# Kernel tuning notes

Measured on AMD Instinct MI355X. Metric: run time of the kernel, lower is better.

Reference implementation:

```python
import jax, jax.numpy as jnp
import numpy as np


def setup_inputs() -> dict:
    key = jax.random.key(0)
    k1, k2, k3, k4 = jax.random.split(key, 4)
    B, S, IN, OUT = 4, 2048, 4096, 4096
    x = jax.random.normal(k1, (B, S, IN), dtype=jnp.float32)
    # 4-bit signed range [-8, 7], stored widened (torch uses int8)
    weight_quantized = jax.random.randint(k2, (OUT, IN), -8, 8, dtype=jnp.int32)
    # per-output-row scale, positive and small (abs-max / 7 style)
    weight_scale = jax.random.uniform(k3, (OUT,), dtype=jnp.float32) * 0.01 + 1e-4
    bias = jax.random.normal(k4, (OUT,), dtype=jnp.float32) * 0.01
    return {"x": x, "weight_quantized": weight_quantized,
            "weight_scale": weight_scale, "bias": bias}


def reference(x, weight_quantized, weight_scale, bias):
    # dequantize: [OUT, IN] int -> fp32 scaled per output row
    w = weight_quantized.astype(jnp.float32) * weight_scale[:, None]
    # F.linear: x @ w.T + bias  -> [B, S, OUT]
    out = jnp.einsum('bsi,oi->bso', x, w) + bias
    return out
```

## Files before the change

### kernel.cpp

```cpp
#include <hip/hip_runtime.h>
#include <hip/hip_bf16.h>

typedef __bf16 bf16x4 __attribute__((ext_vector_type(4)));
typedef __bf16 bf16x8 __attribute__((ext_vector_type(8)));
typedef float  floatx4 __attribute__((ext_vector_type(4)));

#define AS1 __attribute__((address_space(1)))
#define AS3 __attribute__((address_space(3)))

__global__ __launch_bounds__(256)
void cvt_both8(const float* __restrict__ xin, const int* __restrict__ win,
               __bf16* __restrict__ xout, __bf16* __restrict__ wout,
               int nx8, int nw8)
{
    const int stride = gridDim.x * 256;
    const int total  = nx8 + nw8;
    for (int i = blockIdx.x * 256 + threadIdx.x; i < total; i += stride) {
        if (i < nx8) {
            const float4* p = reinterpret_cast<const float4*>(xin) + (size_t)i * 2;
            float4 a = p[0], b = p[1];
            bf16x8 h;
            h[0] = (__bf16)a.x; h[1] = (__bf16)a.y; h[2] = (__bf16)a.z; h[3] = (__bf16)a.w;
            h[4] = (__bf16)b.x; h[5] = (__bf16)b.y; h[6] = (__bf16)b.z; h[7] = (__bf16)b.w;
            reinterpret_cast<bf16x8*>(xout)[i] = h;
        } else {
            int j = i - nx8;
            const int4* p = reinterpret_cast<const int4*>(win) + (size_t)j * 2;
            int4 a = p[0], b = p[1];
            bf16x8 h;
            h[0] = (__bf16)(float)a.x; h[1] = (__bf16)(float)a.y;
            h[2] = (__bf16)(float)a.z; h[3] = (__bf16)(float)a.w;
            h[4] = (__bf16)(float)b.x; h[5] = (__bf16)(float)b.y;
            h[6] = (__bf16)(float)b.z; h[7] = (__bf16)(float)b.w;
            reinterpret_cast<bf16x8*>(wout)[j] = h;
        }
    }
}

#define BM2 256
#define BN2 256
#define BK2 64

template<int P>
__device__ __forceinline__ void phaseAB(const __bf16* cA, const bf16x8 (&bfr)[4][2],
                                        floatx4 (&acc)[8][4],
                                        int wm, int lm, int kq, int sw)
{
    bf16x8 af[2][2];
#pragma unroll
    for (int ii = 0; ii < 2; ++ii)
#pragma unroll
        for (int h = 0; h < 2; ++h)
            af[ii][h] = *reinterpret_cast<const bf16x8*>(
                &cA[(wm + (2 * P + ii) * 16 + lm) * BK2 + ((kq + h * 4) ^ sw) * 8]);
    __builtin_amdgcn_s_setprio(1);
#pragma unroll
    for (int h = 0; h < 2; ++h)
#pragma unroll
        for (int ii = 0; ii < 2; ++ii)
#pragma unroll
            for (int j = 0; j < 4; ++j)
                acc[2 * P + ii][j] = __builtin_amdgcn_mfma_f32_16x16x32_bf16(
                                         af[ii][h], bfr[j][h], acc[2 * P + ii][j], 0, 0, 0);
    __builtin_amdgcn_s_setprio(0);
}

__device__ __forceinline__ void phase3(const __bf16* cA, const __bf16* cBn,
                                       const bf16x8 (&bfr)[4][2], bf16x8 (&bfrN)[4][2],
                                       floatx4 (&acc)[8][4],
                                       int wm, int wn, int lm, int kq, int sw)
{
    bf16x8 af[2][2];
#pragma unroll
    for (int ii = 0; ii < 2; ++ii)
#pragma unroll
        for (int h = 0; h < 2; ++h)
            af[ii][h] = *reinterpret_cast<const bf16x8*>(
                &cA[(wm + (6 + ii) * 16 + lm) * BK2 + ((kq + h * 4) ^ sw) * 8]);
#pragma unroll
    for (int j = 0; j < 4; ++j)
#pragma unroll
        for (int h = 0; h < 2; ++h)
            bfrN[j][h] = *reinterpret_cast<const bf16x8*>(
                &cBn[(wn + j * 16 + lm) * BK2 + ((kq + h * 4) ^ sw) * 8]);
    __builtin_amdgcn_s_setprio(1);
#pragma unroll
    for (int h = 0; h < 2; ++h)
#pragma unroll
        for (int ii = 0; ii < 2; ++ii)
#pragma unroll
            for (int j = 0; j < 4; ++j)
                acc[6 + ii][j] = __builtin_amdgcn_mfma_f32_16x16x32_bf16(
                                     af[ii][h], bfr[j][h], acc[6 + ii][j], 0, 0, 0);
    __builtin_amdgcn_s_setprio(0);
}

#define BARRIER() asm volatile("s_barrier" ::: "memory")

__global__ __launch_bounds__(512)
void gemm_bf16_bt_pipe(const __bf16* __restrict__ A, const __bf16* __restrict__ B,
                       const float* __restrict__ scale, const float* __restrict__ bias,
                       float* __restrict__ Out, int M, int N, int K)
{
    __shared__ __bf16 sA[2][BM2 * BK2];
    __shared__ __bf16 sB[2][BN2 * BK2];

    const int tid  = threadIdx.x;
    const int wave = tid >> 6;
    const int lane = tid & 63;
    const int row0 = blockIdx.y * BM2;
    const int col0 = blockIdx.x * BN2;

    const int sRow = lane >> 3;
    const int gBlk = (lane & 7) ^ sRow;
    const size_t aBase = (size_t)(row0 + wave * 8 + sRow) * K + gBlk * 8;
    const size_t bBase = (size_t)(col0 + wave * 8 + sRow) * K + gBlk * 8;
    const int ldsWOff = wave * 8 * BK2;

#define STAGE_A(buf, q, kt_) \
    __builtin_amdgcn_global_load_lds( \
        (const AS1 void*)(A + aBase + (size_t)(q) * 64 * K + (size_t)(kt_) * BK2), \
        (AS3 void*)&sA[(buf)][(q) * 64 * BK2 + ldsWOff], 16, 0, 0)
#define STAGE_B(buf, q, kt_) \
    __builtin_amdgcn_global_load_lds( \
        (const AS1 void*)(B + bBase + (size_t)(q) * 64 * K + (size_t)(kt_) * BK2), \
        (AS3 void*)&sB[(buf)][(q) * 64 * BK2 + ldsWOff], 16, 0, 0)

    const int wm = (wave >> 2) * 128;
    const int wn = (wave & 3) * 64;
    const int lm = lane & 15;
    const int kq = lane >> 4;
    const int sw = lm & 7;

    floatx4 acc[8][4];
#pragma unroll
    for (int i = 0; i < 8; ++i)
#pragma unroll
        for (int j = 0; j < 4; ++j)
            acc[i][j] = (floatx4)0.0f;

    bf16x8 bfrA[4][2], bfrB[4][2];
    const int nt = K / BK2;

    STAGE_A(0, 0, 0); STAGE_A(0, 1, 0); STAGE_A(0, 2, 0); STAGE_A(0, 3, 0);
    STAGE_B(0, 0, 0); STAGE_B(0, 1, 0); STAGE_B(0, 2, 0); STAGE_B(0, 3, 0);
    STAGE_B(1, 0, 1); STAGE_B(1, 1, 1); STAGE_B(1, 2, 1); STAGE_B(1, 3, 1);
    STAGE_A(1, 0, 1); STAGE_A(1, 2, 1);
    asm volatile("s_waitcnt vmcnt(6)" ::: "memory");
    BARRIER();
#pragma unroll
    for (int j = 0; j < 4; ++j)
#pragma unroll
        for (int h = 0; h < 2; ++h)
            bfrA[j][h] = *reinterpret_cast<const bf16x8*>(
                &sB[0][(wn + j * 16 + lm) * BK2 + ((kq + h * 4) ^ sw) * 8]);

    for (int it = 0; it < nt / 2; ++it) {
        const int kt = 2 * it;
        const int n1 = kt + 1;
        const int n2 = (kt + 2 < nt) ? kt + 2 : 0;
        const int n3 = (kt + 3 < nt) ? kt + 3 : 0;

        STAGE_A(1, 1, n1); STAGE_A(1, 3, n1);
        phaseAB<0>(sA[0], bfrA, acc, wm, lm, kq, sw);
        BARRIER();
        STAGE_B(0, 0, n2); STAGE_B(0, 1, n2); STAGE_B(0, 2, n2); STAGE_B(0, 3, n2);
        phaseAB<1>(sA[0], bfrA, acc, wm, lm, kq, sw);
        BARRIER();
        STAGE_A(0, 0, n2); STAGE_A(0, 2, n2);
        phaseAB<2>(sA[0], bfrA, acc, wm, lm, kq, sw);
        asm volatile("s_waitcnt vmcnt(8)" ::: "memory");
        BARRIER();
        phase3(sA[0], sB[1], bfrA, bfrB, acc, wm, wn, lm, kq, sw);
        BARRIER();

        STAGE_A(0, 1, n2); STAGE_A(0, 3, n2);
        phaseAB<0>(sA[1], bfrB, acc, wm, lm, kq, sw);
        BARRIER();
        STAGE_B(1, 0, n3); STAGE_B(1, 1, n3); STAGE_B(1, 2, n3); STAGE_B(1, 3, n3);
        phaseAB<1>(sA[1], bfrB, acc, wm, lm, kq, sw);
        BARRIER();
        STAGE_A(1, 0, n3); STAGE_A(1, 2, n3);
        phaseAB<2>(sA[1], bfrB, acc, wm, lm, kq, sw);
        asm volatile("s_waitcnt vmcnt(8)" ::: "memory");
        BARRIER();
        phase3(sA[1], sB[0], bfrB, bfrA, acc, wm, wn, lm, kq, sw);
        BARRIER();
    }
    asm volatile("s_waitcnt vmcnt(0)" ::: "memory");

#pragma unroll
    for (int j = 0; j < 4; ++j) {
        int n = col0 + wn + j * 16 + lm;
        float sc = scale[n];
        float bi = bias[n];
#pragma unroll
        for (int i = 0; i < 8; ++i) {
#pragma unroll
            for (int r = 0; r < 4; ++r) {
                int m = row0 + wm + i * 16 + kq * 4 + r;
                Out[(size_t)m * N + n] = sc * acc[i][j][r] + bi;
            }
        }
    }
#undef STAGE_A
#undef STAGE_B
}

#define BM 128
#define BN 128
#define BK 64

__global__ __launch_bounds__(256)
void gemm_bf16_bt(const __bf16* __restrict__ A, const __bf16* __restrict__ B,
                  const float* __restrict__ scale, const float* __restrict__ bias,
                  float* __restrict__ Out, int M, int N, int K)
{
    __shared__ __bf16 sA[BM * BK];
    __shared__ __bf16 sB[BN * BK];

    const int tid  = threadIdx.x;
    const int row0 = blockIdx.y * BM;
    const int col0 = blockIdx.x * BN;
    const int wave = tid >> 6;
    const int lane = tid & 63;

    const int sRow = lane >> 3;
    const int gBlk = (lane & 7) ^ sRow;
    size_t aOff[4], bOff[4];
    const __bf16* ldsA[4];
    const __bf16* ldsB[4];
#pragma unroll
    for (int q = 0; q < 4; ++q) {
        int r = wave * 32 + q * 8 + sRow;
        aOff[q] = (size_t)(row0 + r) * K + gBlk * 8;
        bOff[q] = (size_t)(col0 + r) * K + gBlk * 8;
        ldsA[q] = &sA[(wave * 32 + q * 8) * BK];
        ldsB[q] = &sB[(wave * 32 + q * 8) * BK];
    }

    const int wm = (wave >> 1) * 64;
    const int wn = (wave & 1) * 64;
    const int lm = lane & 15;
    const int kq = lane >> 4;
    const int sw = lm & 7;

    floatx4 acc[4][4];
#pragma unroll
    for (int i = 0; i < 4; ++i)
#pragma unroll
        for (int j = 0; j < 4; ++j)
            acc[i][j] = (floatx4)0.0f;

    for (int k0 = 0; k0 < K; k0 += BK) {
#pragma unroll
        for (int q = 0; q < 4; ++q) {
            __builtin_amdgcn_global_load_lds((const AS1 void*)(A + aOff[q] + k0),
                                             (AS3 void*)ldsA[q], 16, 0, 0);
            __builtin_amdgcn_global_load_lds((const AS1 void*)(B + bOff[q] + k0),
                                             (AS3 void*)ldsB[q], 16, 0, 0);
        }
        __syncthreads();

#pragma unroll
        for (int h = 0; h < 2; ++h) {
            const int blkA = (kq + h * 4);
            bf16x8 af[4], bfr[4];
#pragma unroll
            for (int i = 0; i < 4; ++i) {
                int row = wm + i * 16 + lm;
                af[i] = *reinterpret_cast<const bf16x8*>(
                            &sA[row * BK + (blkA ^ sw) * 8]);
            }
#pragma unroll
            for (int j = 0; j < 4; ++j) {
                int row = wn + j * 16 + lm;
                bfr[j] = *reinterpret_cast<const bf16x8*>(
                            &sB[row * BK + (blkA ^ sw) * 8]);
            }
#pragma unroll
            for (int i = 0; i < 4; ++i)
#pragma unroll
                for (int j = 0; j < 4; ++j)
                    acc[i][j] = __builtin_amdgcn_mfma_f32_16x16x32_bf16(
                                    af[i], bfr[j], acc[i][j], 0, 0, 0);
        }
        __syncthreads();
    }

#pragma unroll
    for (int j = 0; j < 4; ++j) {
        int n = col0 + wn + j * 16 + lm;
        float sc = scale[n];
        float bi = bias[n];
#pragma unroll
        for (int i = 0; i < 4; ++i) {
#pragma unroll
            for (int r = 0; r < 4; ++r) {
                int m = row0 + wm + i * 16 + kq * 4 + r;
                Out[(size_t)m * N + n] = sc * acc[i][j][r] + bi;
            }
        }
    }
}

__global__ __launch_bounds__(256)
void fp4linear_gemm(const float* __restrict__ X, const int* __restrict__ W,
                    const float* __restrict__ scale, const float* __restrict__ bias,
                    float* __restrict__ Out, int M, int N, int K)
{
    __shared__ __bf16 sA[BM * 32];
    __shared__ __bf16 sB[BN * 32];

    const int tid  = threadIdx.x;
    const int row0 = blockIdx.y * BM;
    const int col0 = blockIdx.x * BN;
    const int wave = tid >> 6;
    const int lane = tid & 63;
    const int wm = (wave >> 1) * 64;
    const int wn = (wave & 1) * 64;
    const int lm = lane & 15;
    const int kq = lane >> 4;

    floatx4 acc[4][4];
#pragma unroll
    for (int i = 0; i < 4; ++i)
#pragma unroll
        for (int j = 0; j < 4; ++j)
            acc[i][j] = (floatx4)0.0f;

    for (int k0 = 0; k0 < K; k0 += 32) {
        float4 fa[4];
        int4   ib[4];
#pragma unroll
        for (int l = 0; l < 4; ++l) {
            int idx = tid + l * 256;
            int r = idx >> 3, c4 = idx & 7;
            fa[l] = *reinterpret_cast<const float4*>(
                        &X[(size_t)(row0 + r) * K + k0 + c4 * 4]);
        }
#pragma unroll
        for (int l = 0; l < 4; ++l) {
            int idx = tid + l * 256;
            int r = idx >> 3, c4 = idx & 7;
            ib[l] = *reinterpret_cast<const int4*>(
                        &W[(size_t)(col0 + r) * K + k0 + c4 * 4]);
        }
        __syncthreads();
#pragma unroll
        for (int l = 0; l < 4; ++l) {
            int idx = tid + l * 256;
            int r = idx >> 3, c4 = idx & 7;
            bf16x4 h;
            h[0] = (__bf16)fa[l].x; h[1] = (__bf16)fa[l].y;
            h[2] = (__bf16)fa[l].z; h[3] = (__bf16)fa[l].w;
            *reinterpret_cast<bf16x4*>(&sA[r * 32 + c4 * 4]) = h;
        }
#pragma unroll
        for (int l = 0; l < 4; ++l) {
            int idx = tid + l * 256;
            int r = idx >> 3, c4 = idx & 7;
            bf16x4 h;
            h[0] = (__bf16)(float)ib[l].x; h[1] = (__bf16)(float)ib[l].y;
            h[2] = (__bf16)(float)ib[l].z; h[3] = (__bf16)(float)ib[l].w;
            *reinterpret_cast<bf16x4*>(&sB[r * 32 + c4 * 4]) = h;
        }
        __syncthreads();

        bf16x8 af[4], bfr[4];
#pragma unroll
        for (int i = 0; i < 4; ++i)
            af[i] = *reinterpret_cast<const bf16x8*>(
                        &sA[(wm + i * 16 + lm) * 32 + kq * 8]);
#pragma unroll
        for (int j = 0; j < 4; ++j)
            bfr[j] = *reinterpret_cast<const bf16x8*>(
                        &sB[(wn + j * 16 + lm) * 32 + kq * 8]);
#pragma unroll
        for (int i = 0; i < 4; ++i)
#pragma unroll
            for (int j = 0; j < 4; ++j)
                acc[i][j] = __builtin_amdgcn_mfma_f32_16x16x32_bf16(
                                af[i], bfr[j], acc[i][j], 0, 0, 0);
    }

#pragma unroll
    for (int j = 0; j < 4; ++j) {
        int n = col0 + wn + j * 16 + lm;
        float sc = scale[n];
        float bi = bias[n];
#pragma unroll
        for (int i = 0; i < 4; ++i) {
#pragma unroll
            for (int r = 0; r < 4; ++r) {
                int m = row0 + wm + i * 16 + kq * 4 + r;
                Out[(size_t)m * N + n] = sc * acc[i][j][r] + bi;
            }
        }
    }
}

extern "C" void kernel_launch(void* const* d_in, const int* in_sizes, int n_in,
                              void* d_out, int out_size, void* d_ws, size_t ws_size,
                              hipStream_t stream) {
    const float* x     = (const float*)d_in[0];
    const int*   wq    = (const int*)d_in[1];
    const float* scale = (const float*)d_in[2];
    const float* bias  = (const float*)d_in[3];
    float* out = (float*)d_out;

    const int N = in_sizes[2];
    const int K = in_sizes[1] / N;
    const int M = in_sizes[0] / K;

    const size_t xElems = (size_t)M * K;
    const size_t wElems = (size_t)N * K;
    const size_t need   = (xElems + wElems) * sizeof(__bf16);

    const bool cvt_ok = (ws_size >= need) && (xElems % 8 == 0) && (wElems % 8 == 0);
    const int  nt     = K / BK2;

    if (cvt_ok) {
        __bf16* xb = (__bf16*)d_ws;
        __bf16* wb = xb + xElems;
        int nx8 = (int)(xElems / 8);
        int nw8 = (int)(wElems / 8);
        int total = nx8 + nw8;
        int cvtBlocks = (total + 255) / 256;
        if (cvtBlocks > 2048) cvtBlocks = 2048;
        hipLaunchKernelGGL(cvt_both8, dim3(cvtBlocks), dim3(256), 0, stream,
                           x, wq, xb, wb, nx8, nw8);
        if ((M % BM2 == 0) && (N % BN2 == 0) && (K % BK2 == 0) &&
            (nt % 2 == 0) && (nt >= 4)) {
            hipLaunchKernelGGL(gemm_bf16_bt_pipe, dim3(N / BN2, M / BM2), dim3(512),
                               0, stream, xb, wb, scale, bias, out, M, N, K);
        } else if ((M % BM == 0) && (N % BN == 0) && (K % BK == 0)) {
            hipLaunchKernelGGL(gemm_bf16_bt, dim3(N / BN, M / BM), dim3(256),
                               0, stream, xb, wb, scale, bias, out, M, N, K);
        } else {
            hipLaunchKernelGGL(fp4linear_gemm, dim3(N / BN, M / BM), dim3(256),
                               0, stream, x, wq, scale, bias, out, M, N, K);
        }
    } else {
        hipLaunchKernelGGL(fp4linear_gemm, dim3(N / BN, M / BM), dim3(256), 0, stream,
                           x, wq, scale, bias, out, M, N, K);
    }
}
```

Measured before the change: 532.2 us.

## Prefetch A fragments one phase ahead and rebalance staged loads in pipelined GEMM

Restructures the 256x256 pipelined bf16 GEMM main loop so each phase's MFMA cluster uses A fragments read in the previous phase. The next A fragment set is read from LDS right after the current cluster, with even/odd register sets. It also reorders the prologue staging and adds an extra vmcnt wait per tile to fit the new schedule. The aim is to hide LDS read latency behind MFMA work, at the cost of more live registers and a changed wait/barrier pattern that could stall or hurt occupancy.

```diff
diff --git a/kernel.cpp b/kernel.cpp
--- a/kernel.cpp
+++ b/kernel.cpp
@@ -41,18 +41,13 @@
 #define BN2 256
 #define BK2 64
 
+#define BARRIER() asm volatile("s_barrier" ::: "memory")
+
 template<int P>
-__device__ __forceinline__ void phaseAB(const __bf16* cA, const bf16x8 (&bfr)[4][2],
-                                        floatx4 (&acc)[8][4],
-                                        int wm, int lm, int kq, int sw)
-{
-    bf16x8 af[2][2];
-#pragma unroll
-    for (int ii = 0; ii < 2; ++ii)
-#pragma unroll
-        for (int h = 0; h < 2; ++h)
-            af[ii][h] = *reinterpret_cast<const bf16x8*>(
-                &cA[(wm + (2 * P + ii) * 16 + lm) * BK2 + ((kq + h * 4) ^ sw) * 8]);
+__device__ __forceinline__ void mfma_cluster(floatx4 (&acc)[8][4],
+                                             const bf16x8 (&af)[2][2],
+                                             const bf16x8 (&bfr)[4][2])
+{
     __builtin_amdgcn_s_setprio(1);
 #pragma unroll
     for (int h = 0; h < 2; ++h)
@@ -61,41 +56,31 @@
 #pragma unroll
             for (int j = 0; j < 4; ++j)
                 acc[2 * P + ii][j] = __builtin_amdgcn_mfma_f32_16x16x32_bf16(
-                                         af[ii][h], bfr[j][h], acc[2 * P + ii][j], 0, 0, 0);
+                    af[ii][h], bfr[j][h], acc[2 * P + ii][j], 0, 0, 0);
     __builtin_amdgcn_s_setprio(0);
 }
 
-__device__ __forceinline__ void phase3(const __bf16* cA, const __bf16* cBn,
-                                       const bf16x8 (&bfr)[4][2], bf16x8 (&bfrN)[4][2],
-                                       floatx4 (&acc)[8][4],
-                                       int wm, int wn, int lm, int kq, int sw)
-{
-    bf16x8 af[2][2];
+__device__ __forceinline__ void read_af(bf16x8 (&dst)[2][2], const __bf16* cA,
+                                        int rowBase, int lm, int kq, int sw)
+{
 #pragma unroll
     for (int ii = 0; ii < 2; ++ii)
 #pragma unroll
         for (int h = 0; h < 2; ++h)
-            af[ii][h] = *reinterpret_cast<const bf16x8*>(
-                &cA[(wm + (6 + ii) * 16 + lm) * BK2 + ((kq + h * 4) ^ sw) * 8]);
+            dst[ii][h] = *reinterpret_cast<const bf16x8*>(
+                &cA[(rowBase + ii * 16 + lm) * BK2 + ((kq + h * 4) ^ sw) * 8]);
+}
+
+__device__ __forceinline__ void read_bf(bf16x8 (&dst)[4][2], const __bf16* cB,
+                                        int wn, int lm, int kq, int sw)
+{
 #pragma unroll
     for (int j = 0; j < 4; ++j)
 #pragma unroll
         for (int h = 0; h < 2; ++h)
-            bfrN[j][h] = *reinterpret_cast<const bf16x8*>(
-                &cBn[(wn + j * 16 + lm) * BK2 + ((kq + h * 4) ^ sw) * 8]);
-    __builtin_amdgcn_s_setprio(1);
-#pragma unroll
-    for (int h = 0; h < 2; ++h)
-#pragma unroll
-        for (int ii = 0; ii < 2; ++ii)
-#pragma unroll
-            for (int j = 0; j < 4; ++j)
-                acc[6 + ii][j] = __builtin_amdgcn_mfma_f32_16x16x32_bf16(
-                                     af[ii][h], bfr[j][h], acc[6 + ii][j], 0, 0, 0);
-    __builtin_amdgcn_s_setprio(0);
-}
-
-#define BARRIER() asm volatile("s_barrier" ::: "memory")
+            dst[j][h] = *reinterpret_cast<const bf16x8*>(
+                &cB[(wn + j * 16 + lm) * BK2 + ((kq + h * 4) ^ sw) * 8]);
+}
 
 __global__ __launch_bounds__(512)
 void gemm_bf16_bt_pipe(const __bf16* __restrict__ A, const __bf16* __restrict__ B,
@@ -139,55 +124,58 @@
         for (int j = 0; j < 4; ++j)
             acc[i][j] = (floatx4)0.0f;
 
-    bf16x8 bfrA[4][2], bfrB[4][2];
+    bf16x8 bfr[4][2];
+    bf16x8 afE[2][2];
+    bf16x8 afO[2][2];
     const int nt = K / BK2;
 
-    STAGE_A(0, 0, 0); STAGE_A(0, 1, 0); STAGE_A(0, 2, 0); STAGE_A(0, 3, 0);
+    STAGE_A(0, 0, 0); STAGE_A(0, 2, 0);
     STAGE_B(0, 0, 0); STAGE_B(0, 1, 0); STAGE_B(0, 2, 0); STAGE_B(0, 3, 0);
+    STAGE_A(0, 1, 0); STAGE_A(0, 3, 0);
     STAGE_B(1, 0, 1); STAGE_B(1, 1, 1); STAGE_B(1, 2, 1); STAGE_B(1, 3, 1);
     STAGE_A(1, 0, 1); STAGE_A(1, 2, 1);
-    asm volatile("s_waitcnt vmcnt(6)" ::: "memory");
+    asm volatile("s_waitcnt vmcnt(8)" ::: "memory");
     BARRIER();
-#pragma unroll
-    for (int j = 0; j < 4; ++j)
-#pragma unroll
-        for (int h = 0; h < 2; ++h)
-            bfrA[j][h] = *reinterpret_cast<const bf16x8*>(
-                &sB[0][(wn + j * 16 + lm) * BK2 + ((kq + h * 4) ^ sw) * 8]);
+    read_bf(bfr, sB[0], wn, lm, kq, sw);
+    read_af(afE, sA[0], wm, lm, kq, sw);
+
+#define TILE(c, n1, n2)                                                        \
+                                                                       \
+    STAGE_A((c) ^ 1, 1, n1); STAGE_A((c) ^ 1, 3, n1);                          \
+    mfma_cluster<0>(acc, afE, bfr);                                            \
+    read_af(afO, sA[(c)], wm + 32, lm, kq, sw);                                \
+    asm volatile("s_waitcnt vmcnt(8)" ::: "memory");                           \
+    BARRIER();                                                                 \
+                                                                       \
+    STAGE_B((c), 0, n2); STAGE_B((c), 1, n2);                                  \
+    STAGE_B((c), 2, n2); STAGE_B((c), 3, n2);                                  \
+    mfma_cluster<1>(acc, afO, bfr);                                            \
+    read_af(afE, sA[(c)], wm + 64, lm, kq, sw);                                \
+    BARRIER();                                                                 \
+                                                                       \
+    STAGE_A((c), 0, n2); STAGE_A((c), 2, n2);                                  \
+    mfma_cluster<2>(acc, afE, bfr);                                            \
+    read_af(afO, sA[(c)], wm + 96, lm, kq, sw);                                \
+    asm volatile("s_waitcnt vmcnt(8)" ::: "memory");                           \
+    BARRIER();                                                                 \
+                                                                       \
+    mfma_cluster<3>(acc, afO, bfr);                                            \
+    read_bf(bfr, sB[(c) ^ 1], wn, lm, kq, sw);                                 \
+    read_af(afE, sA[(c) ^ 1], wm, lm, kq, sw);                                 \
+    BARRIER();
 
     for (int it = 0; it < nt / 2; ++it) {
         const int kt = 2 * it;
-        const int n1 = kt + 1;
-        const int n2 = (kt + 2 < nt) ? kt + 2 : 0;
-        const int n3 = (kt + 3 < nt) ? kt + 3 : 0;
-
-        STAGE_A(1, 1, n1); STAGE_A(1, 3, n1);
-        phaseAB<0>(sA[0], bfrA, acc, wm, lm, kq, sw);
-        BARRIER();
-        STAGE_B(0, 0, n2); STAGE_B(0, 1, n2); STAGE_B(0, 2, n2); STAGE_B(0, 3, n2);
-        phaseAB<1>(sA[0], bfrA, acc, wm, lm, kq, sw);
-        BARRIER();
-        STAGE_A(0, 0, n2); STAGE_A(0, 2, n2);
-        phaseAB<2>(sA[0], bfrA, acc, wm, lm, kq, sw);
-        asm volatile("s_waitcnt vmcnt(8)" ::: "memory");
-        BARRIER();
-        phase3(sA[0], sB[1], bfrA, bfrB, acc, wm, wn, lm, kq, sw);
-        BARRIER();
-
-        STAGE_A(0, 1, n2); STAGE_A(0, 3, n2);
-        phaseAB<0>(sA[1], bfrB, acc, wm, lm, kq, sw);
-        BARRIER();
-        STAGE_B(1, 0, n3); STAGE_B(1, 1, n3); STAGE_B(1, 2, n3); STAGE_B(1, 3, n3);
-        phaseAB<1>(sA[1], bfrB, acc, wm, lm, kq, sw);
-        BARRIER();
-        STAGE_A(1, 0, n3); STAGE_A(1, 2, n3);
-        phaseAB<2>(sA[1], bfrB, acc, wm, lm, kq, sw);
-        asm volatile("s_waitcnt vmcnt(8)" ::: "memory");
-        BARRIER();
-        phase3(sA[1], sB[0], bfrB, bfrA, acc, wm, wn, lm, kq, sw);
-        BARRIER();
+        const int e1 = kt + 1;
+        const int e2 = (kt + 2 < nt) ? kt + 2 : 0;
+        const int o2 = (kt + 3 < nt) ? kt + 3 : 0;
+        TILE(0, e1, e2)
+        TILE(1, e2, o2)
     }
     asm volatile("s_waitcnt vmcnt(0)" ::: "memory");
+#undef TILE
+#undef STAGE_A
+#undef STAGE_B
 
 #pragma unroll
     for (int j = 0; j < 4; ++j) {
@@ -203,8 +191,6 @@
             }
         }
     }
-#undef STAGE_A
-#undef STAGE_B
 }
 
 #define BM 128
```

New measurement: 507.0 us. 1.05x faster.
